# Kernel tuning notes

Measured on AMD Instinct MI355X. Metric: run time of the kernel, lower is better.

Reference implementation:

```python
import math
import jax, jax.numpy as jnp
from jax import lax
import numpy as np

STRIDES = (8, 16, 32)            # p3, p4, p5
ANCHOR_STRIDE_SCALE = 8
ASPECT_RATIOS = (0.5, 1.0, 2.0)  # A = 3
NMS_THRESH = 0.6
PRE_NMS_TOPK = 400
POST_NMS_TOPK = 50
BBOX_CLAMP = 4.135166556742356   # log(1000/16)


def setup_inputs() -> dict:
    key = jax.random.key(0)
    ks = jax.random.split(key, 8)
    C = 256
    inp = {
        "p3": jax.random.normal(ks[0], (8, C, 128, 128), jnp.float32),
        "p4": jax.random.normal(ks[1], (8, C, 64, 64), jnp.float32),
        "p5": jax.random.normal(ks[2], (8, C, 32, 32), jnp.float32),
        # fan-in scaled weights so logits/deltas stay in a sane range
        "w_stem": jax.random.normal(ks[3], (C, C, 3, 3), jnp.float32) * (1.0 / math.sqrt(C * 9)),
        "b_stem": jnp.zeros((C,), jnp.float32),
        "w_obj": jax.random.normal(ks[4], (3, C, 1, 1), jnp.float32) * (1.0 / math.sqrt(C)),
        "b_obj": jnp.zeros((3,), jnp.float32),
        "w_box": jax.random.normal(ks[5], (12, C, 1, 1), jnp.float32) * (0.01 / math.sqrt(C)),
        "b_box": jnp.zeros((12,), jnp.float32),
    }
    return inp


def _conv(x, w, b, pad):
    y = lax.conv_general_dilated(x, w, (1, 1), pad,
                                 dimension_numbers=("NCHW", "OIHW", "NCHW"))
    return y + b[None, :, None, None]


def _make_anchors(H, W, stride):
    # anchor centers at (x+0.5)*stride ; base size = stride * anchor_stride_scale
    xs = (jnp.arange(W, dtype=jnp.float32) + 0.5) * stride
    ys = (jnp.arange(H, dtype=jnp.float32) + 0.5) * stride
    cx, cy = jnp.meshgrid(xs, ys)              # (H, W), row-major matches H*W flatten
    cx = cx.reshape(-1)
    cy = cy.reshape(-1)
    size = float(stride * ANCHOR_STRIDE_SCALE)
    per_ratio = []
    for r in ASPECT_RATIOS:
        w = size / math.sqrt(r)
        h = size * math.sqrt(r)
        per_ratio.append(jnp.stack([cx - w / 2, cy - h / 2, cx + w / 2, cy + h / 2], axis=-1))
    return jnp.stack(per_ratio, axis=1).reshape(-1, 4)  # (H*W*A, 4)


def _decode(deltas, anchors):
    aw = anchors[:, 2] - anchors[:, 0]
    ah = anchors[:, 3] - anchors[:, 1]
    acx = anchors[:, 0] + 0.5 * aw
    acy = anchors[:, 1] + 0.5 * ah
    dx, dy = deltas[:, 0], deltas[:, 1]
    dw = jnp.clip(deltas[:, 2], -BBOX_CLAMP, BBOX_CLAMP)
    dh = jnp.clip(deltas[:, 3], -BBOX_CLAMP, BBOX_CLAMP)
    pcx = acx + dx * aw
    pcy = acy + dy * ah
    pw = aw * jnp.exp(dw)
    ph = ah * jnp.exp(dh)
    return jnp.stack([pcx - 0.5 * pw, pcy - 0.5 * ph,
                      pcx + 0.5 * pw, pcy + 0.5 * ph], axis=-1)


def _nms_keep(boxes, thresh):
    # boxes already sorted by descending score; greedy class-agnostic NMS
    N = boxes.shape[0]
    x1, y1, x2, y2 = boxes[:, 0], boxes[:, 1], boxes[:, 2], boxes[:, 3]
    area = jnp.maximum(x2 - x1, 0.0) * jnp.maximum(y2 - y1, 0.0)
    ix1 = jnp.maximum(x1[:, None], x1[None, :])
    iy1 = jnp.maximum(y1[:, None], y1[None, :])
    ix2 = jnp.minimum(x2[:, None], x2[None, :])
    iy2 = jnp.minimum(y2[:, None], y2[None, :])
    inter = jnp.maximum(ix2 - ix1, 0.0) * jnp.maximum(iy2 - iy1, 0.0)
    iou = inter / jnp.maximum(area[:, None] + area[None, :] - inter, 1e-8)  # (N, N)
    idx = jnp.arange(N)

    def body(keep, i):
        suppress = (iou[i] > thresh) & keep[i] & (idx > i)
        return keep & ~suppress, 0

    keep, _ = lax.scan(body, jnp.ones((N,), bool), idx)
    return keep


def _proposals_one_image(logits, deltas, anchors):
    # logits: (N,), deltas: (N, 4), anchors: (N, 4)
    k = min(PRE_NMS_TOPK, logits.shape[0])
    scores, top_idx = lax.top_k(logits, k)
    boxes = _decode(deltas[top_idx], anchors[top_idx])
    keep = _nms_keep(boxes, NMS_THRESH)
    masked = jnp.where(keep, scores, -jnp.inf)
    _, kidx = lax.top_k(masked, POST_NMS_TOPK)
    return boxes[kidx]  # (POST_NMS_TOPK, 4)


def _rpn_level(feat, w_stem, b_stem, w_obj, b_obj, w_box, b_box, stride):
    B, _, H, W = feat.shape
    x = jax.nn.relu(_conv(feat, w_stem, b_stem, "SAME"))       # stem: 3x3 conv + ReLU
    obj = _conv(x, w_obj, b_obj, "VALID")                      # (B, A, H, W)
    box = _conv(x, w_box, b_box, "VALID")                      # (B, 4A, H, W)
    A = obj.shape[1]
    obj = obj.transpose(0, 2, 3, 1).reshape(B, H * W * A)       # (B, HWA)
    box = box.transpose(0, 2, 3, 1).reshape(B, H * W * A, 4)    # (B, HWA, 4)
    anchors = _make_anchors(H, W, stride)                       # (HWA, 4)
    return jax.vmap(lambda o, d: _proposals_one_image(o, d, anchors))(obj, box)


def reference(p3, p4, p5, w_stem, b_stem, w_obj, b_obj, w_box, b_box):
    out = []
    for feat, stride in zip((p3, p4, p5), STRIDES):
        out.append(_rpn_level(feat, w_stem, b_stem, w_obj, b_obj, w_box, b_box, stride))
    # (B, 3 * POST_NMS_TOPK, 4) absolute XYXY proposals, concatenated across levels
    return jnp.concatenate(out, axis=1)
```

## Files before the change

kernel.cpp:

```cpp
#include <hip/hip_runtime.h>
#include <math.h>
#include <stdint.h>

#define BBOX_CLAMP 4.135166556742356f
#define SQH 0.70710678118654752f
#define SQ2 1.41421356237309515f

typedef __attribute__((ext_vector_type(8))) short s8b;
typedef __attribute__((ext_vector_type(4))) float f32x4;
typedef __attribute__((ext_vector_type(4))) short s4b;

__device__ __forceinline__ unsigned okey(float f){
  unsigned u = __float_as_uint(f);
  return (u & 0x80000000u) ? ~u : (u | 0x80000000u);
}
__device__ __forceinline__ unsigned short f2bf(float f){
  unsigned u = __float_as_uint(f);
  unsigned r = (u + 0x7FFFu + ((u >> 16) & 1u)) >> 16;
  return (unsigned short)r;
}
__device__ __forceinline__ float bf2f(unsigned short h){
  return __uint_as_float(((unsigned)h) << 16);
}

__global__ void k_wsplit(const float* __restrict__ w,
                         unsigned short* __restrict__ whi, unsigned short* __restrict__ wlo){
  const int ck = blockIdx.x;
  const int cout = threadIdx.x;
  const int cin = ck / 9, tap = ck - cin*9;
  const float x = w[cout*2304 + ck];
  const unsigned short h = f2bf(x);
  const unsigned short lo2 = f2bf(x - bf2f(h));
  const int slice = cin >> 5, g = (cin >> 3) & 3, j = cin & 7;
  const size_t off = ((((size_t)tap*8 + slice)*4 + g)*256 + cout)*8 + j;
  whi[off] = h; wlo[off] = lo2;
}

__global__ __launch_bounds__(256, 2) void k_stem_mfma(
    const float* __restrict__ p3f, const float* __restrict__ p4f, const float* __restrict__ p5f,
    const unsigned short* __restrict__ whi, const unsigned short* __restrict__ wlo,
    const float* __restrict__ bstem,
    const float* __restrict__ wobj, const float* __restrict__ bobj,
    const float* __restrict__ wbox, const float* __restrict__ bbox,
    float* __restrict__ sc3, float* __restrict__ dl3,
    float* __restrict__ sc4, float* __restrict__ dl4,
    float* __restrict__ sc5, float* __restrict__ dl5)
{
  __shared__ __align__(16) unsigned char smem[21760];
  unsigned short* Abuf = reinterpret_cast<unsigned short*>(smem);
  float* part = reinterpret_cast<float*>(smem);

  const int tid = threadIdx.x;
  const int l = tid & 63, w = tid >> 6;
  const int li = l & 15, g = l >> 4;
  const int p = w >> 1, c = w & 1;

  int id = blockIdx.x;
  const float* feat; float* scores; float* deltas; int H, W, bx, by, b;
  if (id < 2048){ feat=p3f; scores=sc3; deltas=dl3; H=128; W=128;
      bx = id & 3; by = (id >> 2) & 63; b = id >> 8; }
  else if (id < 2560){ id -= 2048; feat=p4f; scores=sc4; deltas=dl4; H=64; W=64;
      bx = id & 1; by = (id >> 1) & 31; b = id >> 6; }
  else { id -= 2560; feat=p5f; scores=sc5; deltas=dl5; H=32; W=32;
      bx = 0; by = id & 15; b = id >> 4; }
  const int px0 = bx*32, py0 = by*2;
  const size_t HW = (size_t)H*W;
  const float* fb = feat + (size_t)b*256*HW;

  const int gr = tid / 34, gc = tid - gr*34;
  const int row = py0 + gr - 1, col = px0 + gc - 1;
  const bool lact = (tid < 136);
  const bool inb = lact && row >= 0 && row < H && col >= 0 && col < W;
  const float* gA = fb + ((size_t)(inb ? row : 0)*W + (inb ? col : 0));

  f32x4 acc[2][8];
#pragma unroll
  for (int m=0;m<2;++m)
#pragma unroll
    for (int cg=0;cg<8;++cg) acc[m][cg] = (f32x4){0.f,0.f,0.f,0.f};

  for (int slice = 0; slice < 8; ++slice){
    __syncthreads();
    const float* gs = gA + (size_t)slice*32*HW;
#pragma unroll 2
    for (int ch = 0; ch < 8; ++ch){
      float x0=0.f, x1=0.f, x2=0.f, x3=0.f;
      if (inb){
        x0 = gs[(size_t)(ch*4+0)*HW];
        x1 = gs[(size_t)(ch*4+1)*HW];
        x2 = gs[(size_t)(ch*4+2)*HW];
        x3 = gs[(size_t)(ch*4+3)*HW];
      }
      if (lact){
        const unsigned short h0=f2bf(x0), h1=f2bf(x1), h2=f2bf(x2), h3=f2bf(x3);
        s4b hv; hv[0]=(short)h0; hv[1]=(short)h1; hv[2]=(short)h2; hv[3]=(short)h3;
        s4b lv; lv[0]=(short)f2bf(x0-bf2f(h0)); lv[1]=(short)f2bf(x1-bf2f(h1));
                lv[2]=(short)f2bf(x2-bf2f(h2)); lv[3]=(short)f2bf(x3-bf2f(h3));
        *reinterpret_cast<s4b*>(&Abuf[tid*40 + ch*4]) = hv;
        *reinterpret_cast<s4b*>(&Abuf[5440 + tid*40 + ch*4]) = lv;
      }
    }
    __syncthreads();

    for (int tap = 0; tap < 9; ++tap){
      const int dr = tap/3 - 1, dc = tap - (tap/3)*3 - 1;
      s8b ah[2], al[2];
#pragma unroll
      for (int m = 0; m < 2; ++m){
        const int aoff = ((p+dr+1)*34 + m*16 + li + dc + 1)*40 + g*8;
        ah[m] = *reinterpret_cast<const s8b*>(&Abuf[aoff]);
        al[m] = *reinterpret_cast<const s8b*>(&Abuf[5440 + aoff]);
      }
#pragma unroll
      for (int chunk = 0; chunk < 4; ++chunk){
        s8b bh[2], bl[2];
#pragma unroll
        for (int cg2 = 0; cg2 < 2; ++cg2){
          const int cout = c*128 + (chunk*2 + cg2)*16 + li;
          const int woff = ((((tap*8 + slice)*4 + g)*256) + cout)*8;
          bh[cg2] = *reinterpret_cast<const s8b*>(&whi[woff]);
          bl[cg2] = *reinterpret_cast<const s8b*>(&wlo[woff]);
        }
#pragma unroll
        for (int m = 0; m < 2; ++m){
#pragma unroll
          for (int cg2 = 0; cg2 < 2; ++cg2)
            acc[m][chunk*2+cg2] = __builtin_amdgcn_mfma_f32_16x16x32_bf16(ah[m], bh[cg2], acc[m][chunk*2+cg2], 0, 0, 0);
#pragma unroll
          for (int cg2 = 0; cg2 < 2; ++cg2)
            acc[m][chunk*2+cg2] = __builtin_amdgcn_mfma_f32_16x16x32_bf16(ah[m], bl[cg2], acc[m][chunk*2+cg2], 0, 0, 0);
#pragma unroll
          for (int cg2 = 0; cg2 < 2; ++cg2)
            acc[m][chunk*2+cg2] = __builtin_amdgcn_mfma_f32_16x16x32_bf16(al[m], bh[cg2], acc[m][chunk*2+cg2], 0, 0, 0);
        }
      }
    }
  }

#pragma unroll
  for (int cg = 0; cg < 8; ++cg){
    const float bsv = bstem[c*128 + cg*16 + li];
#pragma unroll
    for (int m = 0; m < 2; ++m)
#pragma unroll
      for (int r = 0; r < 4; ++r)
        acc[m][cg][r] = fmaxf(acc[m][cg][r] + bsv, 0.f);
  }

  __syncthreads();

#pragma unroll
  for (int oc = 0; oc < 15; ++oc){
    float wv[8];
#pragma unroll
    for (int cg = 0; cg < 8; ++cg){
      const int cc = c*128 + cg*16 + li;
      wv[cg] = (oc < 3) ? wobj[oc*256 + cc] : wbox[(oc-3)*256 + cc];
    }
#pragma unroll
    for (int m = 0; m < 2; ++m){
#pragma unroll
      for (int r = 0; r < 4; ++r){
        float t = acc[m][0][r] * wv[0];
#pragma unroll
        for (int cg = 1; cg < 8; ++cg) t = fmaf(acc[m][cg][r], wv[cg], t);
        t += __shfl_xor(t, 1, 64);
        t += __shfl_xor(t, 2, 64);
        t += __shfl_xor(t, 4, 64);
        t += __shfl_xor(t, 8, 64);
        if (li == 0)
          part[(w*32 + m*16 + g*4 + r)*17 + oc] = t;
      }
    }
  }
  __syncthreads();

  if (tid < 128){
    const int px = tid & 63, half = tid >> 6;
    const int rw = px >> 5, cl = px & 31;
    const int hh = py0 + rw, ww = px0 + cl;
    const size_t loc = (size_t)hh*W + ww;
    const int oce = half ? 15 : 8;
    for (int oc = half*8; oc < oce; ++oc){
      float s = part[((rw*2 + 0)*32 + cl)*17 + oc]
              + part[((rw*2 + 1)*32 + cl)*17 + oc];
      s += (oc < 3) ? bobj[oc] : bbox[oc-3];
      if (oc < 3) scores[(size_t)b*HW*3 + loc*3 + oc] = s;
      else        deltas[(size_t)b*HW*12 + loc*12 + (oc-3)] = s;
    }
  }
}

__global__ __launch_bounds__(1024) void k_select(
    const float* __restrict__ sc3, const float* __restrict__ sc4, const float* __restrict__ sc5,
    const float* __restrict__ dl3, const float* __restrict__ dl4, const float* __restrict__ dl5,
    float* __restrict__ out)
{
  const int lvl = blockIdx.x >> 3;
  const int b   = blockIdx.x & 7;
  int N, W; float stride; const float* sc; const float* dl;
  if (lvl==0){ N=49152; W=128; stride=8.f;  sc=sc3; dl=dl3; }
  else if (lvl==1){ N=12288; W=64; stride=16.f; sc=sc4; dl=dl4; }
  else { N=3072; W=32; stride=32.f; sc=sc5; dl=dl5; }
  sc += (size_t)b*N;
  dl += (size_t)b*(size_t)(N/3)*12;

  __shared__ unsigned hist[256];
  __shared__ unsigned s_prefix;
  __shared__ int s_need;
  __shared__ int s_cntc;
  __shared__ unsigned long long cand[1024];
  __shared__ int tk[400];
  __shared__ float bx1[400], by1[400], bx2[400], by2[400], bar_[400];
  __shared__ unsigned long long mask[400][7];
  __shared__ int olist[50];

  const int t = threadIdx.x;

  if (t==0){ s_prefix=0u; s_need=400; }
  for (int pass=0; pass<4; ++pass){
    const int shift = 24 - 8*pass;
    if (t<256) hist[t]=0u;
    __syncthreads();
    const unsigned pref = s_prefix;
    for (int i=t; i<N; i+=1024){
      const unsigned k = okey(sc[i]);
      if (pass==0 || (k >> (shift+8)) == pref)
        atomicAdd(&hist[(k>>shift)&255u], 1u);
    }
    __syncthreads();
    if (t==0){
      int need = s_need, cum=0, bsel=0;
      for (int bb=255; bb>=0; --bb){
        const int h = (int)hist[bb];
        if (cum + h >= need){ bsel=bb; break; }
        cum += h;
      }
      s_prefix = (pref<<8) | (unsigned)bsel;
      s_need = need - cum;
    }
    __syncthreads();
  }
  const unsigned K = s_prefix;

  if (t==0) s_cntc = 0;
  cand[t] = 0ull;
  __syncthreads();
  for (int i=t; i<N; i+=1024){
    const unsigned k = okey(sc[i]);
    if (k >= K){
      const int pos = atomicAdd(&s_cntc, 1);
      if (pos < 1024)
        cand[pos] = ((unsigned long long)k<<32) | (unsigned long long)(0xFFFFFFFFu - (unsigned)i);
    }
  }
  __syncthreads();

  for (int kk=2; kk<=1024; kk<<=1){
    for (int j=kk>>1; j>0; j>>=1){
      const int ixj = t ^ j;
      if (ixj > t){
        const unsigned long long a = cand[t], c = cand[ixj];
        const bool descending = ((t & kk) == 0);
        if ((a < c) == descending){ cand[t]=c; cand[ixj]=a; }
      }
      __syncthreads();
    }
  }

  if (t < 400){
    const unsigned long long c = cand[t];
    const int gi = (int)(0xFFFFFFFFu - (unsigned)(c & 0xFFFFFFFFull));
    tk[t] = gi;
    const int loc = gi/3, a = gi - loc*3;
    const int hh = loc / W, ww = loc - hh*W;
    const float cx = (ww + 0.5f)*stride, cy = (hh + 0.5f)*stride;
    const float size = stride*8.f;
    const float sq = (a==0) ? SQH : ((a==1) ? 1.f : SQ2);
    const float hw_ = 0.5f*(size/sq);
    const float hv_ = 0.5f*(size*sq);
    const float ax1 = cx - hw_, ax2 = cx + hw_;
    const float ay1 = cy - hv_, ay2 = cy + hv_;
    const float aw = ax2 - ax1, ah = ay2 - ay1;
    const float acx = ax1 + 0.5f*aw, acy = ay1 + 0.5f*ah;
    const float* dd = dl + (size_t)loc*12 + a*4;
    const float dx = dd[0], dy = dd[1];
    const float dw = fminf(fmaxf(dd[2], -BBOX_CLAMP), BBOX_CLAMP);
    const float dh = fminf(fmaxf(dd[3], -BBOX_CLAMP), BBOX_CLAMP);
    const float pcx = acx + dx*aw;
    const float pcy = acy + dy*ah;
    const float pw = aw*expf(dw);
    const float ph = ah*expf(dh);
    const float x1 = pcx - 0.5f*pw, y1 = pcy - 0.5f*ph;
    const float x2 = pcx + 0.5f*pw, y2 = pcy + 0.5f*ph;
    bx1[t]=x1; by1[t]=y1; bx2[t]=x2; by2[t]=y2;
    bar_[t] = fmaxf(x2-x1, 0.f)*fmaxf(y2-y1, 0.f);
  }
  __syncthreads();

  for (int task=t; task<2800; task+=1024){
    const int i = task/7, w = task - (task/7)*7;
    unsigned long long m = 0ull;
    const float xi1=bx1[i], yi1=by1[i], xi2=bx2[i], yi2=by2[i], ai=bar_[i];
    const int j0 = w<<6;
    const int js = (j0 > i+1) ? j0 : (i+1);
    const int je = (j0+64 < 400) ? (j0+64) : 400;
    for (int j=js; j<je; ++j){
      const float ix1 = fmaxf(xi1, bx1[j]);
      const float iy1 = fmaxf(yi1, by1[j]);
      const float ix2 = fminf(xi2, bx2[j]);
      const float iy2 = fminf(yi2, by2[j]);
      const float inter = fmaxf(ix2-ix1, 0.f)*fmaxf(iy2-iy1, 0.f);
      const float iou = inter / fmaxf(ai + bar_[j] - inter, 1e-8f);
      if (iou > 0.6f) m |= (1ull << (j - j0));
    }
    mask[i][w] = m;
  }
  __syncthreads();

  if (t==0){
    unsigned long long keepw[7];
#pragma unroll
    for (int w=0;w<7;++w) keepw[w] = ~0ull;
    for (int i=0;i<400;++i){
      if ((keepw[i>>6] >> (i&63)) & 1ull){
#pragma unroll
        for (int w=0;w<7;++w) keepw[w] &= ~mask[i][w];
      }
    }
    int cnt=0;
    for (int i=0;i<400 && cnt<50;++i) if ( (keepw[i>>6]>>(i&63)) & 1ull) olist[cnt++]=i;
    for (int i=0;i<400 && cnt<50;++i) if (!((keepw[i>>6]>>(i&63)) & 1ull)) olist[cnt++]=i;
  }
  __syncthreads();

  if (t < 50){
    const int j = olist[t];
    float* o = out + (size_t)b*600 + (size_t)(lvl*50 + t)*4;
    o[0]=bx1[j]; o[1]=by1[j]; o[2]=bx2[j]; o[3]=by2[j];
  }
}

extern "C" void kernel_launch(void* const* d_in, const int* in_sizes, int n_in,
                              void* d_out, int out_size, void* d_ws, size_t ws_size,
                              hipStream_t stream) {
  (void)in_sizes; (void)n_in; (void)out_size; (void)ws_size;
  const float* p3     = (const float*)d_in[0];
  const float* p4     = (const float*)d_in[1];
  const float* p5     = (const float*)d_in[2];
  const float* w_stem = (const float*)d_in[3];
  const float* b_stem = (const float*)d_in[4];
  const float* w_obj  = (const float*)d_in[5];
  const float* b_obj  = (const float*)d_in[6];
  const float* w_box  = (const float*)d_in[7];
  const float* b_box  = (const float*)d_in[8];
  float* out = (float*)d_out;

  unsigned short* whi = (unsigned short*)d_ws;
  unsigned short* wlo = whi + 589824;
  float* sc3 = (float*)(wlo + 589824);
  float* sc4 = sc3 + 393216;
  float* sc5 = sc4 + 98304;
  float* dl3 = sc5 + 24576;
  float* dl4 = dl3 + 1572864;
  float* dl5 = dl4 + 393216;

  k_wsplit<<<dim3(2304), dim3(256), 0, stream>>>(w_stem, whi, wlo);

  k_stem_mfma<<<dim3(2688), dim3(256), 0, stream>>>(
      p3, p4, p5, whi, wlo, b_stem, w_obj, b_obj, w_box, b_box,
      sc3, dl3, sc4, dl4, sc5, dl5);

  k_select<<<dim3(24), dim3(1024), 0, stream>>>(sc3, sc4, sc5, dl3, dl4, dl5, out);
}
```

Baseline: 839.5 us.

## Pre-convert features to channel-sliced NHWC bf16 hi/lo before stem conv

Adds a transpose kernel that converts each NCHW fp32 feature map into a 32-channel-sliced NHWC layout, already split into bf16 hi and lo parts, held in workspace. The stem MFMA kernel then loads its halo tile with contiguous 16-byte vector reads and no per-element conversion, instead of gathering strided fp32 values and splitting them itself. The cost is an extra full read and write pass over all features, plus a large workspace requirement. A fallback to the old kernel is kept for when the workspace is too small.

```diff
diff --git a/kernel.cpp b/kernel.cpp
--- a/kernel.cpp
+++ b/kernel.cpp
@@ -36,7 +36,204 @@
   whi[off] = h; wlo[off] = lo2;
 }
 
-__global__ __launch_bounds__(256, 2) void k_stem_mfma(
+__global__ __launch_bounds__(256) void k_aconv(
+    const float* __restrict__ in, unsigned short* __restrict__ out,
+    const int H, const int W)
+{
+  __shared__ float t[32][33];
+  const int tid = threadIdx.x;
+  const int col0 = blockIdx.x*32;
+  const int row = blockIdx.y;
+  const int z = blockIdx.z;
+  const int bb = z >> 3, s = z & 7;
+  const size_t HW = (size_t)H*W;
+
+  {
+    const int col = tid & 31, cl = tid >> 5;
+#pragma unroll
+    for (int i = 0; i < 4; ++i){
+      const int cin = cl + i*8;
+      t[cin][col] = in[((size_t)(bb*256 + s*32 + cin))*HW + (size_t)row*W + col0 + col];
+    }
+  }
+  __syncthreads();
+  {
+    const int c5 = tid & 31, colg = tid >> 5;
+    const size_t robase = (((size_t)z*2 + 0)*H + row)*(size_t)W;
+    const size_t robase1 = (((size_t)z*2 + 1)*H + row)*(size_t)W;
+#pragma unroll
+    for (int i = 0; i < 4; ++i){
+      const int col = colg + i*8;
+      const float x = t[c5][col];
+      const unsigned short h = f2bf(x);
+      out[(robase  + col0 + col)*32 + c5] = h;
+      out[(robase1 + col0 + col)*32 + c5] = f2bf(x - bf2f(h));
+    }
+  }
+}
+
+__global__ __launch_bounds__(256, 2) void k_stem_nhwc(
+    const unsigned short* __restrict__ a3, const unsigned short* __restrict__ a4,
+    const unsigned short* __restrict__ a5,
+    const unsigned short* __restrict__ whi, const unsigned short* __restrict__ wlo,
+    const float* __restrict__ bstem,
+    const float* __restrict__ wobj, const float* __restrict__ bobj,
+    const float* __restrict__ wbox, const float* __restrict__ bbox,
+    float* __restrict__ sc3, float* __restrict__ dl3,
+    float* __restrict__ sc4, float* __restrict__ dl4,
+    float* __restrict__ sc5, float* __restrict__ dl5)
+{
+  __shared__ __align__(16) unsigned char smem[21760];
+  unsigned short* Abuf = reinterpret_cast<unsigned short*>(smem);
+  float* part = reinterpret_cast<float*>(smem);
+
+  const int tid = threadIdx.x;
+  const int l = tid & 63, w = tid >> 6;
+  const int li = l & 15, g = l >> 4;
+  const int p = w >> 1, c = w & 1;
+
+  int id = blockIdx.x;
+  const unsigned short* Alvl; float* scores; float* deltas; int H, W, bx, by, b;
+  if (id < 2048){ Alvl=a3; scores=sc3; deltas=dl3; H=128; W=128;
+      bx = id & 3; by = (id >> 2) & 63; b = id >> 8; }
+  else if (id < 2560){ id -= 2048; Alvl=a4; scores=sc4; deltas=dl4; H=64; W=64;
+      bx = id & 1; by = (id >> 1) & 31; b = id >> 6; }
+  else { id -= 2560; Alvl=a5; scores=sc5; deltas=dl5; H=32; W=32;
+      bx = 0; by = id & 15; b = id >> 4; }
+  const int px0 = bx*32, py0 = by*2;
+  const size_t HW = (size_t)H*W;
+  const size_t sstep = (size_t)2*HW*32;
+
+  const int pl0 = (tid >= 136) ? 1 : 0;
+  const int pos0 = tid - pl0*136;
+  const int gr0 = pos0/34, gc0 = pos0 - gr0*34;
+  const int row0 = py0+gr0-1, col0 = px0+gc0-1;
+  const bool v0 = (row0>=0 && row0<H && col0>=0 && col0<W);
+  const unsigned short* s0 = Alvl + ((((size_t)(b*8+0)*2 + pl0)*H + (v0?row0:0))*(size_t)W + (v0?col0:0))*32;
+  unsigned short* d0 = Abuf + pl0*5440 + pos0*40;
+  const bool has2 = (tid < 16);
+  const int pos1 = 120 + tid;
+  const int gr1 = pos1/34, gc1 = pos1 - gr1*34;
+  const int row1 = py0+gr1-1, col1 = px0+gc1-1;
+  const bool v1 = has2 && (row1>=0 && row1<H && col1>=0 && col1<W);
+  const unsigned short* s1 = Alvl + ((((size_t)(b*8+0)*2 + 1)*H + (v1?row1:0))*(size_t)W + (v1?col1:0))*32;
+  unsigned short* d1 = Abuf + 5440 + pos1*40;
+
+  f32x4 acc[2][8];
+#pragma unroll
+  for (int m=0;m<2;++m)
+#pragma unroll
+    for (int cg=0;cg<8;++cg) acc[m][cg] = (f32x4){0.f,0.f,0.f,0.f};
+
+  for (int slice = 0; slice < 8; ++slice){
+    __syncthreads();
+    {
+      const s8b z8 = {0,0,0,0,0,0,0,0};
+      const s8b* sp = reinterpret_cast<const s8b*>(s0 + slice*sstep);
+      s8b q0=z8,q1=z8,q2=z8,q3=z8;
+      if (v0){ q0=sp[0]; q1=sp[1]; q2=sp[2]; q3=sp[3]; }
+      *reinterpret_cast<s8b*>(d0+ 0)=q0; *reinterpret_cast<s8b*>(d0+ 8)=q1;
+      *reinterpret_cast<s8b*>(d0+16)=q2; *reinterpret_cast<s8b*>(d0+24)=q3;
+      if (has2){
+        const s8b* sq = reinterpret_cast<const s8b*>(s1 + slice*sstep);
+        s8b r0=z8,r1=z8,r2=z8,r3=z8;
+        if (v1){ r0=sq[0]; r1=sq[1]; r2=sq[2]; r3=sq[3]; }
+        *reinterpret_cast<s8b*>(d1+ 0)=r0; *reinterpret_cast<s8b*>(d1+ 8)=r1;
+        *reinterpret_cast<s8b*>(d1+16)=r2; *reinterpret_cast<s8b*>(d1+24)=r3;
+      }
+    }
+    __syncthreads();
+
+    for (int tap = 0; tap < 9; ++tap){
+      const int dr = tap/3 - 1, dc = tap - (tap/3)*3 - 1;
+      s8b ah[2], al[2];
+#pragma unroll
+      for (int m = 0; m < 2; ++m){
+        const int aoff = ((p+dr+1)*34 + m*16 + li + dc + 1)*40 + g*8;
+        ah[m] = *reinterpret_cast<const s8b*>(&Abuf[aoff]);
+        al[m] = *reinterpret_cast<const s8b*>(&Abuf[5440 + aoff]);
+      }
+#pragma unroll
+      for (int chunk = 0; chunk < 4; ++chunk){
+        s8b bh[2], bl[2];
+#pragma unroll
+        for (int cg2 = 0; cg2 < 2; ++cg2){
+          const int cout = c*128 + (chunk*2 + cg2)*16 + li;
+          const int woff = ((((tap*8 + slice)*4 + g)*256) + cout)*8;
+          bh[cg2] = *reinterpret_cast<const s8b*>(&whi[woff]);
+          bl[cg2] = *reinterpret_cast<const s8b*>(&wlo[woff]);
+        }
+#pragma unroll
+        for (int m = 0; m < 2; ++m){
+#pragma unroll
+          for (int cg2 = 0; cg2 < 2; ++cg2)
+            acc[m][chunk*2+cg2] = __builtin_amdgcn_mfma_f32_16x16x32_bf16(ah[m], bh[cg2], acc[m][chunk*2+cg2], 0, 0, 0);
+#pragma unroll
+          for (int cg2 = 0; cg2 < 2; ++cg2)
+            acc[m][chunk*2+cg2] = __builtin_amdgcn_mfma_f32_16x16x32_bf16(ah[m], bl[cg2], acc[m][chunk*2+cg2], 0, 0, 0);
+#pragma unroll
+          for (int cg2 = 0; cg2 < 2; ++cg2)
+            acc[m][chunk*2+cg2] = __builtin_amdgcn_mfma_f32_16x16x32_bf16(al[m], bh[cg2], acc[m][chunk*2+cg2], 0, 0, 0);
+        }
+      }
+    }
+  }
+
+#pragma unroll
+  for (int cg = 0; cg < 8; ++cg){
+    const float bsv = bstem[c*128 + cg*16 + li];
+#pragma unroll
+    for (int m = 0; m < 2; ++m)
+#pragma unroll
+      for (int r = 0; r < 4; ++r)
+        acc[m][cg][r] = fmaxf(acc[m][cg][r] + bsv, 0.f);
+  }
+
+  __syncthreads();
+
+#pragma unroll
+  for (int oc = 0; oc < 15; ++oc){
+    float wv[8];
+#pragma unroll
+    for (int cg = 0; cg < 8; ++cg){
+      const int cc = c*128 + cg*16 + li;
+      wv[cg] = (oc < 3) ? wobj[oc*256 + cc] : wbox[(oc-3)*256 + cc];
+    }
+#pragma unroll
+    for (int m = 0; m < 2; ++m){
+#pragma unroll
+      for (int r = 0; r < 4; ++r){
+        float t = acc[m][0][r] * wv[0];
+#pragma unroll
+        for (int cg = 1; cg < 8; ++cg) t = fmaf(acc[m][cg][r], wv[cg], t);
+        t += __shfl_xor(t, 1, 64);
+        t += __shfl_xor(t, 2, 64);
+        t += __shfl_xor(t, 4, 64);
+        t += __shfl_xor(t, 8, 64);
+        if (li == 0)
+          part[(w*32 + m*16 + g*4 + r)*17 + oc] = t;
+      }
+    }
+  }
+  __syncthreads();
+
+  if (tid < 128){
+    const int px = tid & 63, half = tid >> 6;
+    const int rw = px >> 5, cl = px & 31;
+    const int hh = py0 + rw, ww = px0 + cl;
+    const size_t loc = (size_t)hh*W + ww;
+    const int oce = half ? 15 : 8;
+    for (int oc = half*8; oc < oce; ++oc){
+      float s = part[((rw*2 + 0)*32 + cl)*17 + oc]
+              + part[((rw*2 + 1)*32 + cl)*17 + oc];
+      s += (oc < 3) ? bobj[oc] : bbox[oc-3];
+      if (oc < 3) scores[(size_t)b*HW*3 + loc*3 + oc] = s;
+      else        deltas[(size_t)b*HW*12 + loc*12 + (oc-3)] = s;
+    }
+  }
+}
+
+__global__ __launch_bounds__(256, 2) void k_stem_old(
     const float* __restrict__ p3f, const float* __restrict__ p4f, const float* __restrict__ p5f,
     const unsigned short* __restrict__ whi, const unsigned short* __restrict__ wlo,
     const float* __restrict__ bstem,
@@ -344,7 +541,7 @@
 extern "C" void kernel_launch(void* const* d_in, const int* in_sizes, int n_in,
                               void* d_out, int out_size, void* d_ws, size_t ws_size,
                               hipStream_t stream) {
-  (void)in_sizes; (void)n_in; (void)out_size; (void)ws_size;
+  (void)in_sizes; (void)n_in; (void)out_size;
   const float* p3     = (const float*)d_in[0];
   const float* p4     = (const float*)d_in[1];
   const float* p5     = (const float*)d_in[2];
@@ -364,12 +561,27 @@
   float* dl3 = sc5 + 24576;
   float* dl4 = dl3 + 1572864;
   float* dl5 = dl4 + 393216;
+  unsigned short* a3 = (unsigned short*)(dl5 + 98304);
+  unsigned short* a4 = a3 + 67108864;
+  unsigned short* a5 = a4 + 16777216;
+
+  const size_t need = 2359296ull + 10321920ull + 176160768ull;
+  const bool fast = (ws_size >= need);
 
   k_wsplit<<<dim3(2304), dim3(256), 0, stream>>>(w_stem, whi, wlo);
 
-  k_stem_mfma<<<dim3(2688), dim3(256), 0, stream>>>(
-      p3, p4, p5, whi, wlo, b_stem, w_obj, b_obj, w_box, b_box,
-      sc3, dl3, sc4, dl4, sc5, dl5);
+  if (fast){
+    k_aconv<<<dim3(4, 128, 64), dim3(256), 0, stream>>>(p3, a3, 128, 128);
+    k_aconv<<<dim3(2,  64, 64), dim3(256), 0, stream>>>(p4, a4,  64,  64);
+    k_aconv<<<dim3(1,  32, 64), dim3(256), 0, stream>>>(p5, a5,  32,  32);
+    k_stem_nhwc<<<dim3(2688), dim3(256), 0, stream>>>(
+        a3, a4, a5, whi, wlo, b_stem, w_obj, b_obj, w_box, b_box,
+        sc3, dl3, sc4, dl4, sc5, dl5);
+  } else {
+    k_stem_old<<<dim3(2688), dim3(256), 0, stream>>>(
+        p3, p4, p5, whi, wlo, b_stem, w_obj, b_obj, w_box, b_box,
+        sc3, dl3, sc4, dl4, sc5, dl5);
+  }
 
   k_select<<<dim3(24), dim3(1024), 0, stream>>>(sc3, sc4, sc5, dl3, dl4, dl5, out);
 }
```

After: 895.5 us. +6.7%, slower.
